# Kernel tuning notes

Measured on AMD Instinct MI355X. Metric: run time of the kernel, lower is better.

Reference implementation:

```python
import jax, jax.numpy as jnp
import numpy as np

TIME_CONSTANT = 1.0
VM_THRESHOLD = 2.0
WINDOW = 100          # integration_window
AMPLITUDE = 1.0


def setup_inputs() -> dict:
    key = jax.random.key(0)
    # [B, T, H, W, C] positive drive so integrate-and-fire actually spikes
    inputs = jax.random.uniform(key, (4, 200, 64, 64, 8), dtype=jnp.float32)
    return {"inputs": inputs}


def _process_chunk(chunk):
    """Iterative integrate-and-fire on one time chunk [B, T, H, W, C].
    Each while-iteration extracts one spike per neuron (first threshold
    crossing of the running cumsum), resets the membrane, and zeroes the
    consumed input so the next cumsum restarts after the spike."""
    B, T = chunk.shape[0], chunk.shape[1]
    img = chunk.shape[2:]
    spikes0 = jnp.zeros((B,) + img + (T + 1,), chunk.dtype)
    vout0 = jnp.zeros_like(chunk)

    def body(state):
        ch, vout, spikes, _ = state
        V = jnp.cumsum(ch * TIME_CONSTANT, axis=1)            # membrane potential
        temp = jax.nn.relu(V - VM_THRESHOLD)
        has = jnp.any(temp > 0)                                # any neuron fires?
        ctemp = jnp.cumsum(temp, axis=1)                       # zero before first crossing
        tstar = jnp.sum((ctemp == 0).astype(jnp.int32), axis=1)  # [B,H,W,C] spike time (T => none)
        spikes_new = spikes + jax.nn.one_hot(tstar, T + 1, dtype=ch.dtype)
        rolled = jnp.roll(ctemp, 1, axis=1).at[:, 0].set(0.0)  # nonzero strictly after spike
        mask = rolled == 0
        vout_spk = jnp.where(mask, vout + V, 0.0)              # record V up to spike, reset after
        ch_spk = jnp.where(mask, 0.0, ch)                      # consume input up to spike
        # if no spikes this pass: accumulate residual V and stop (do-while break)
        vout_n = jnp.where(has, vout_spk, vout + V)
        ch_n = jnp.where(has, ch_spk, ch)
        spikes_n = jnp.where(has, spikes_new, spikes)
        return ch_n, vout_n, spikes_n, jnp.logical_not(has)

    def cond(state):
        return jnp.logical_not(state[3])

    state = (chunk, vout0, spikes0, jnp.array(False))
    _, vout, spikes, _ = jax.lax.while_loop(cond, body, state)
    return vout, spikes[..., :T]   # drop the 'no spike' bin


def reference(inputs):
    T = inputs.shape[1]
    sizes = [WINDOW] * (T // WINDOW) + ([T % WINDOW] if T % WINDOW else [])
    spike_chunks = []
    start = 0
    for s in sizes:  # small fixed chunk loop (structural, not a data dim)
        ch = inputs[:, start:start + s]
        start += s
        _, sp = _process_chunk(ch)
        spike_chunks.append(sp)
    spikes = jnp.concatenate(spike_chunks, axis=-1)   # [B, H, W, C, T]
    out = jnp.swapaxes(spikes, 1, -1)                 # [B, T, W, C, H] (as in source)
    if AMPLITUDE != 1.0:
        out = out * AMPLITUDE
    return out
```

## Files before the change

### kernel.cpp

```cpp
#include <hip/hip_runtime.h>
#include <stdint.h>

#define BDIM    4
#define TTOT    200
#define CHUNK   100
#define HWC     32768
#define NEUR    (BDIM * HWC)
#define REGION_BYTES (HWC * 4)

__global__ __launch_bounds__(256) void spike_kernel(const float* __restrict__ x,
                                                    uint8_t* __restrict__ out8) {
    unsigned g     = blockIdx.x * 256u + threadIdx.x;
    unsigned n     = g & (NEUR - 1);
    unsigned chunk = g >> 17;
    unsigned b     = n >> 15;
    unsigned i     = n & (HWC - 1);
    unsigned t0    = b * TTOT + chunk * CHUNK;

    const float* xp = x    + (size_t)t0 * HWC + i;
    uint8_t*     sp = out8 + (size_t)t0 * REGION_BYTES + i;

    float acc = 0.0f;
#pragma unroll 4
    for (int t = 0; t < CHUNK; ++t) {
        float v = xp[(size_t)t * HWC];
        acc += v;
        uint8_t s = 0;
        if (acc > 2.0f) { s = 1; acc = 0.0f; }
        sp[(size_t)t * REGION_BYTES] = s;
    }
}

__global__ __launch_bounds__(256) void transpose_kernel(float* __restrict__ out) {
    __shared__ uint32_t lds32[64 * 129];
    unsigned blk = blockIdx.x;
    unsigned tid = threadIdx.x;

    const uint32_t* in32 = (const uint32_t*)((const uint8_t*)out + (size_t)blk * REGION_BYTES);

#pragma unroll 8
    for (int it = 0; it < 32; ++it) {
        unsigned idx = it * 256u + tid;
        unsigned h   = idx >> 7;
        unsigned wq  = idx & 127u;
        lds32[h * 129u + wq] = in32[idx];
    }
    __syncthreads();

    const uint8_t* lds8 = (const uint8_t*)lds32;
    float4* out4 = (float4*)out + (size_t)blk * 8192u;

#pragma unroll 8
    for (int it = 0; it < 32; ++it) {
        unsigned o4   = it * 256u + tid;
        unsigned oidx = o4 * 4u;
        unsigned wc   = oidx >> 6;
        unsigned h0   = oidx & 63u;
        float4 v;
        v.x = (float)lds8[(h0 + 0u) * 516u + wc];
        v.y = (float)lds8[(h0 + 1u) * 516u + wc];
        v.z = (float)lds8[(h0 + 2u) * 516u + wc];
        v.w = (float)lds8[(h0 + 3u) * 516u + wc];
        out4[o4] = v;
    }
}

extern "C" void kernel_launch(void* const* d_in, const int* in_sizes, int n_in,
                              void* d_out, int out_size, void* d_ws, size_t ws_size,
                              hipStream_t stream) {
    (void)in_sizes; (void)n_in; (void)d_ws; (void)ws_size; (void)out_size;
    const float* x = (const float*)d_in[0];
    float* out = (float*)d_out;

    hipLaunchKernelGGL(spike_kernel, dim3(NEUR * 2 / 256), dim3(256), 0, stream,
                       x, (uint8_t*)out);
    hipLaunchKernelGGL(transpose_kernel, dim3(BDIM * TTOT), dim3(256), 0, stream,
                       out);
}
```

Measured before the change: 187.4 us.

## Stage packed spikes in workspace, vectorize spike loads, split transpose blocks

The spike kernel now handles two neurons per thread with float2 loads and 16-bit stores, halving the thread count. When the workspace is big enough, spikes go into a compact workspace buffer with a 32KB region stride instead of strided slots inside the output, and the transpose reads from there using two blocks per region. A fallback keeps the in-place path, now with 512-thread blocks. The aim is to cut strided, sparse byte traffic and improve coalescing, at the cost of lower parallelism in the spike kernel.

Result: no change. 188.2 us (+0.5%).

```diff
diff --git a/kernel.cpp b/kernel.cpp
--- a/kernel.cpp
+++ b/kernel.cpp
@@ -1,79 +1,121 @@
 #include <hip/hip_runtime.h>
 #include <stdint.h>
 
-#define BDIM    4
-#define TTOT    200
-#define CHUNK   100
-#define HWC     32768
-#define NEUR    (BDIM * HWC)
-#define REGION_BYTES (HWC * 4)
+#define BDIM   4
+#define TTOT   200
+#define CHUNK  100
+#define HWC    32768
+#define NREG   (BDIM * TTOT)
+#define RS_WS  32768u
+#define RS_IP  131072u
 
 __global__ __launch_bounds__(256) void spike_kernel(const float* __restrict__ x,
-                                                    uint8_t* __restrict__ out8) {
+                                                    uint8_t* __restrict__ spk,
+                                                    unsigned rstride) {
     unsigned g     = blockIdx.x * 256u + threadIdx.x;
-    unsigned n     = g & (NEUR - 1);
-    unsigned chunk = g >> 17;
-    unsigned b     = n >> 15;
-    unsigned i     = n & (HWC - 1);
+    unsigned chunk = g >> 16;
+    unsigned p     = g & 65535u;
+    unsigned b     = p >> 14;
+    unsigned i     = (p & 16383u) * 2u;
     unsigned t0    = b * TTOT + chunk * CHUNK;
 
-    const float* xp = x    + (size_t)t0 * HWC + i;
-    uint8_t*     sp = out8 + (size_t)t0 * REGION_BYTES + i;
+    const float2* xp = (const float2*)(x + (size_t)t0 * HWC + i);
+    uint8_t*      sp = spk + (size_t)t0 * rstride + i;
 
-    float acc = 0.0f;
-#pragma unroll 4
-    for (int t = 0; t < CHUNK; ++t) {
-        float v = xp[(size_t)t * HWC];
-        acc += v;
-        uint8_t s = 0;
-        if (acc > 2.0f) { s = 1; acc = 0.0f; }
-        sp[(size_t)t * REGION_BYTES] = s;
+    float a0 = 0.0f, a1 = 0.0f;
+    for (int tb = 0; tb < CHUNK; tb += 4) {
+        float2 v[4];
+#pragma unroll
+        for (int k = 0; k < 4; ++k) v[k] = xp[(size_t)k * (HWC / 2)];
+        xp += 4 * (HWC / 2);
+#pragma unroll
+        for (int k = 0; k < 4; ++k) {
+            a0 += v[k].x; a1 += v[k].y;
+            unsigned s0 = 0u, s1 = 0u;
+            if (a0 > 2.0f) { s0 = 1u; a0 = 0.0f; }
+            if (a1 > 2.0f) { s1 = 1u; a1 = 0.0f; }
+            *(uint16_t*)sp = (uint16_t)(s0 | (s1 << 8));
+            sp += rstride;
+        }
     }
 }
 
-__global__ __launch_bounds__(256) void transpose_kernel(float* __restrict__ out) {
-    __shared__ uint32_t lds32[64 * 129];
+__global__ __launch_bounds__(256) void transpose_ws(const uint8_t* __restrict__ spk,
+                                                    float* __restrict__ out) {
+    __shared__ uint32_t lds[64 * 65];
     unsigned blk = blockIdx.x;
+    unsigned region = blk >> 1, half = blk & 1u;
     unsigned tid = threadIdx.x;
 
-    const uint32_t* in32 = (const uint32_t*)((const uint8_t*)out + (size_t)blk * REGION_BYTES);
-
-#pragma unroll 8
-    for (int it = 0; it < 32; ++it) {
+    const uint32_t* in32 = (const uint32_t*)(spk + (size_t)region * RS_WS);
+#pragma unroll
+    for (int it = 0; it < 16; ++it) {
         unsigned idx = it * 256u + tid;
-        unsigned h   = idx >> 7;
-        unsigned wq  = idx & 127u;
-        lds32[h * 129u + wq] = in32[idx];
+        unsigned h = idx >> 6, wq = idx & 63u;
+        lds[h * 65u + wq] = in32[h * 128u + half * 64u + wq];
     }
     __syncthreads();
 
-    const uint8_t* lds8 = (const uint8_t*)lds32;
-    float4* out4 = (float4*)out + (size_t)blk * 8192u;
+    float4* out4 = (float4*)out + (size_t)region * 8192u + half * 4096u;
+#pragma unroll
+    for (int it = 0; it < 16; ++it) {
+        unsigned f   = it * 256u + tid;
+        unsigned wcl = f >> 4;
+        unsigned h0  = (f & 15u) << 2;
+        unsigned wq  = wcl >> 2, sel = (wcl & 3u) * 8u;
+        float4 v;
+        v.x = (float)((lds[(h0 + 0u) * 65u + wq] >> sel) & 1u);
+        v.y = (float)((lds[(h0 + 1u) * 65u + wq] >> sel) & 1u);
+        v.z = (float)((lds[(h0 + 2u) * 65u + wq] >> sel) & 1u);
+        v.w = (float)((lds[(h0 + 3u) * 65u + wq] >> sel) & 1u);
+        out4[f] = v;
+    }
+}
 
-#pragma unroll 8
-    for (int it = 0; it < 32; ++it) {
-        unsigned o4   = it * 256u + tid;
-        unsigned oidx = o4 * 4u;
-        unsigned wc   = oidx >> 6;
-        unsigned h0   = oidx & 63u;
+__global__ __launch_bounds__(512) void transpose_ip(float* __restrict__ out) {
+    __shared__ uint32_t lds[64 * 129];
+    unsigned region = blockIdx.x;
+    unsigned tid = threadIdx.x;
+
+    const uint32_t* in32 = (const uint32_t*)((const uint8_t*)out + (size_t)region * RS_IP);
+#pragma unroll
+    for (int it = 0; it < 16; ++it) {
+        unsigned idx = it * 512u + tid;
+        unsigned h = idx >> 7, wq = idx & 127u;
+        lds[h * 129u + wq] = in32[idx];
+    }
+    __syncthreads();
+
+    float4* out4 = (float4*)out + (size_t)region * 8192u;
+#pragma unroll
+    for (int it = 0; it < 16; ++it) {
+        unsigned f  = it * 512u + tid;
+        unsigned wc = f >> 4;
+        unsigned h0 = (f & 15u) << 2;
+        unsigned wq = wc >> 2, sel = (wc & 3u) * 8u;
         float4 v;
-        v.x = (float)lds8[(h0 + 0u) * 516u + wc];
-        v.y = (float)lds8[(h0 + 1u) * 516u + wc];
-        v.z = (float)lds8[(h0 + 2u) * 516u + wc];
-        v.w = (float)lds8[(h0 + 3u) * 516u + wc];
-        out4[o4] = v;
+        v.x = (float)((lds[(h0 + 0u) * 129u + wq] >> sel) & 1u);
+        v.y = (float)((lds[(h0 + 1u) * 129u + wq] >> sel) & 1u);
+        v.z = (float)((lds[(h0 + 2u) * 129u + wq] >> sel) & 1u);
+        v.w = (float)((lds[(h0 + 3u) * 129u + wq] >> sel) & 1u);
+        out4[f] = v;
     }
 }
 
 extern "C" void kernel_launch(void* const* d_in, const int* in_sizes, int n_in,
                               void* d_out, int out_size, void* d_ws, size_t ws_size,
                               hipStream_t stream) {
-    (void)in_sizes; (void)n_in; (void)d_ws; (void)ws_size; (void)out_size;
+    (void)in_sizes; (void)n_in; (void)out_size;
     const float* x = (const float*)d_in[0];
     float* out = (float*)d_out;
 
-    hipLaunchKernelGGL(spike_kernel, dim3(NEUR * 2 / 256), dim3(256), 0, stream,
-                       x, (uint8_t*)out);
-    hipLaunchKernelGGL(transpose_kernel, dim3(BDIM * TTOT), dim3(256), 0, stream,
-                       out);
+    const size_t spike_bytes = (size_t)NREG * RS_WS;
+    if (ws_size >= spike_bytes) {
+        uint8_t* spk = (uint8_t*)d_ws;
+        hipLaunchKernelGGL(spike_kernel, dim3(512), dim3(256), 0, stream, x, spk, RS_WS);
+        hipLaunchKernelGGL(transpose_ws, dim3(2 * NREG), dim3(256), 0, stream, spk, out);
+    } else {
+        hipLaunchKernelGGL(spike_kernel, dim3(512), dim3(256), 0, stream, x, (uint8_t*)out, RS_IP);
+        hipLaunchKernelGGL(transpose_ip, dim3(NREG), dim3(512), 0, stream, out);
+    }
 }
```
